# Performance work log

Hardware: AMD Instinct MI355X
Metric: run time of the kernel (lower is better)

The kernel has to match this reference:

```python
import jax, jax.numpy as jnp
import numpy as np

N_NODES = 50000


def gcn_conv(x, src, dst, W, b):
    # PyG GCNConv: h = x @ W; symmetric norm with added self-loops; out = A_hat h + b
    h = x @ W
    deg = jax.ops.segment_sum(jnp.ones_like(src, dtype=h.dtype), dst,
                              num_segments=N_NODES) + 1.0  # +1 self-loop
    dis = jax.lax.rsqrt(deg)  # deg >= 1, safe
    msg = h[src] * (dis[src] * dis[dst])[:, None]          # [E,H] gather + scale
    agg = jax.ops.segment_sum(msg, dst, num_segments=N_NODES)
    agg = agg + h * (dis * dis)[:, None]                   # self-loop contribution
    return agg + b


def link_pred(zs, e, Wp, bp):
    # zs: [L,N,H]; gather endpoints along node dim, per-edge cross-layer Gram matrix
    s = zs[:, e[0]]                                # [L,E,H]
    d = zs[:, e[1]]                                # [L,E,H]
    dot = jnp.einsum('leh,meh->elm', s, d)         # [E,L,L] per-edge bmm
    emb = dot.reshape(dot.shape[0], -1)            # [E,L*L]
    return emb @ Wp + bp                           # [E,1] logits (activation=False)


def reference(x, ei, pos, neg, W0, b0, Wh, bh, Wp, bp):
    src, dst = ei[0], ei[1]
    h = jax.nn.relu(gcn_conv(x, src, dst, W0, b0))
    embs = [h]
    for i in range(Wh.shape[0]):  # fixed small layer count
        h = jax.nn.relu(gcn_conv(h, src, dst, Wh[i], bh[i]))
        embs.append(h)
    zs = jnp.stack(embs, axis=0)                   # [L,N,H]
    pos_pred = link_pred(zs, pos, Wp, bp)
    neg_pred = link_pred(zs, neg, Wp, bp)
    logits = jnp.concatenate([pos_pred, neg_pred], axis=0)  # [2E,1]
    # faithful to source: targets all zero except row index == n_pos set to 1
    targets = jnp.zeros_like(logits).at[pos_pred.shape[0]].set(1.0)
    # BCEWithLogitsLoss (mean, numerically stable)
    loss = jnp.mean(jnp.clip(logits, 0.0) - logits * targets
                    + jnp.log1p(jnp.exp(-jnp.abs(logits))))
    return loss


def setup_inputs():
    key = jax.random.key(0)
    ks = jax.random.split(key, 10)
    N, E, EP, IN, H, L = 50000, 800000, 100000, 128, 64, 4
    x = jax.random.normal(ks[0], (N, IN), jnp.float32)
    ei = jax.random.randint(ks[1], (2, E), 0, N, dtype=jnp.int32)
    pos = jax.random.randint(ks[2], (2, EP), 0, N, dtype=jnp.int32)
    neg = jax.random.randint(ks[3], (2, EP), 0, N, dtype=jnp.int32)
    def u(k, shape, fan_in):
        s = 1.0 / np.sqrt(fan_in)
        return jax.random.uniform(k, shape, jnp.float32, -s, s)
    W0 = u(ks[4], (IN, H), IN)
    b0 = u(ks[5], (H,), IN)
    Wh = u(ks[6], (L - 1, H, H), H)
    bh = u(ks[7], (L - 1, H), H)
    Wp = u(ks[8], (L * L, 1), L * L)
    bp = u(ks[9], (1,), L * L)
    return {"x": x, "ei": ei, "pos": pos, "neg": neg, "W0": W0, "b0": b0,
            "Wh": Wh, "bh": bh, "Wp": Wp, "bp": bp}
```

## Files before the change

### kernel.cpp

```cpp
#include <hip/hip_runtime.h>
#include <hip/hip_bf16.h>
#include <math.h>

constexpr int N_NODES = 50000;
constexpr int HD = 64;
constexpr int NBKT = (N_NODES + 255) / 256;

typedef float floatx2 __attribute__((ext_vector_type(2)));

__device__ __forceinline__ float bf2f(unsigned short u) {
    return __uint_as_float((unsigned)u << 16);
}
__device__ __forceinline__ unsigned short f2bf(float f) {
    __hip_bfloat16 b = __float2bfloat16(f);
    return *(unsigned short*)&b;
}
__device__ __forceinline__ unsigned pack_fp8x4(float a, float b, float c, float d) {
    unsigned p = __builtin_amdgcn_cvt_pk_fp8_f32(a, b, 0u, false);
    return __builtin_amdgcn_cvt_pk_fp8_f32(c, d, p, true);
}
__device__ __forceinline__ float dot16_fp8(uint4 u, uint4 d) {
    const unsigned uu[4] = {u.x, u.y, u.z, u.w};
    const unsigned dd[4] = {d.x, d.y, d.z, d.w};
    float s = 0.f;
#pragma unroll
    for (int q = 0; q < 4; ++q) {
        floatx2 ua = __builtin_amdgcn_cvt_pk_f32_fp8(uu[q], false);
        floatx2 ub = __builtin_amdgcn_cvt_pk_f32_fp8(uu[q], true);
        floatx2 da = __builtin_amdgcn_cvt_pk_f32_fp8(dd[q], false);
        floatx2 db = __builtin_amdgcn_cvt_pk_f32_fp8(dd[q], true);
        s = fmaf(ua[0], da[0], s);
        s = fmaf(ua[1], da[1], s);
        s = fmaf(ub[0], db[0], s);
        s = fmaf(ub[1], db[1], s);
    }
    return s;
}

__global__ __launch_bounds__(256) void gemm128_bhist_kernel(
        const float* __restrict__ in_, const float* __restrict__ W,
        unsigned short* __restrict__ out16, unsigned* __restrict__ out8,
        const int* __restrict__ dst, int* __restrict__ bcnt,
        int N, int E, int nGemm) {
    __shared__ float xs[64][68];
    __shared__ float Wl[64][64];
    const int t = threadIdx.x;
    if ((int)blockIdx.x >= nGemm) {
        int* lh = (int*)&xs[0][0];
        lh[t] = 0;
        __syncthreads();
        const int beg = ((int)blockIdx.x - nGemm) * 2048;
        const int end = min(beg + 2048, E);
        for (int i = beg + t; i < end; i += 256)
            atomicAdd(&lh[dst[i] >> 8], 1);
        __syncthreads();
        if (t < NBKT && lh[t]) atomicAdd(&bcnt[t], lh[t]);
        return;
    }
    constexpr int K = 128;
    const int row0 = blockIdx.x * 64;
    const int cq = t & 15, rq = t >> 4;
    float acc[4][4] = {{0.f}};
    for (int kc = 0; kc < K; kc += 64) {
#pragma unroll
        for (int it = 0; it < 4; ++it) {
            const int idx = it * 256 + t;
            const int r = idx >> 4, c4 = idx & 15;
            const int rr = min(row0 + r, N - 1);
            *(float4*)(&xs[r][c4 * 4]) = *(const float4*)(in_ + (size_t)rr * K + kc + c4 * 4);
            *(float4*)(&Wl[r][c4 * 4]) = *(const float4*)(W + (size_t)(kc + r) * HD + c4 * 4);
        }
        __syncthreads();
#pragma unroll
        for (int k4 = 0; k4 < 16; ++k4) {
            float a[4][4], b[4][4];
#pragma unroll
            for (int i = 0; i < 4; ++i)
                *(float4*)a[i] = *(const float4*)(&xs[rq * 4 + i][k4 * 4]);
#pragma unroll
            for (int kk = 0; kk < 4; ++kk)
                *(float4*)b[kk] = *(const float4*)(&Wl[k4 * 4 + kk][cq * 4]);
#pragma unroll
            for (int kk = 0; kk < 4; ++kk)
#pragma unroll
                for (int i = 0; i < 4; ++i)
#pragma unroll
                    for (int j = 0; j < 4; ++j)
                        acc[i][j] = fmaf(a[i][kk], b[kk][j], acc[i][j]);
        }
        __syncthreads();
    }
#pragma unroll
    for (int i = 0; i < 4; ++i) {
        const int r = row0 + rq * 4 + i;
        if (r < N) {
            ushort4 o;
            o.x = f2bf(acc[i][0]); o.y = f2bf(acc[i][1]);
            o.z = f2bf(acc[i][2]); o.w = f2bf(acc[i][3]);
            *(ushort4*)(out16 + (size_t)r * HD + cq * 4) = o;
            out8[(size_t)r * 16 + cq] = pack_fp8x4(acc[i][0], acc[i][1], acc[i][2], acc[i][3]);
        }
    }
}

__global__ __launch_bounds__(256) void bscan_kernel(const int* __restrict__ bcnt,
                                                    int* __restrict__ bbase,
                                                    int* __restrict__ gcur) {
    const int t = threadIdx.x;
    const int v = (t < NBKT) ? bcnt[t] : 0;
    const int lane = t & 63, wid = t >> 6;
    int incl = v;
#pragma unroll
    for (int o = 1; o <= 32; o <<= 1) {
        int u = __shfl_up(incl, o);
        if (lane >= o) incl += u;
    }
    __shared__ int wt[4];
    if (lane == 63) wt[wid] = incl;
    __syncthreads();
    int base = 0;
    for (int w = 0; w < wid; ++w) base += wt[w];
    const int excl = base + incl - v;
    if (t < NBKT) { bbase[t] = excl; gcur[t] = excl; }
    if (t == NBKT - 1) bbase[NBKT] = excl + v;
}

__global__ __launch_bounds__(256) void partition_kernel(const int* __restrict__ src,
                                                        const int* __restrict__ dst,
                                                        int* __restrict__ gcur,
                                                        unsigned* __restrict__ pk, int E) {
    __shared__ unsigned epk[8192];
    __shared__ int lh[NBKT], lbase[NBKT], lcur[NBKT];
    const int t = threadIdx.x;
    for (int i = t; i < NBKT; i += 256) { lh[i] = 0; lcur[i] = 0; }
    __syncthreads();
    const int beg = blockIdx.x * 8192;
    const int end = min(beg + 8192, E);
    for (int i = beg + t; i < end; i += 256) {
        const int s = src[i], d = dst[i];
        const int bkt = d >> 8;
        epk[i - beg] = ((unsigned)bkt << 24) | ((unsigned)(d & 255) << 16) | (unsigned)s;
        atomicAdd(&lh[bkt], 1);
    }
    __syncthreads();
    for (int i = t; i < NBKT; i += 256)
        if (lh[i]) lbase[i] = atomicAdd(&gcur[i], lh[i]);
    __syncthreads();
    for (int i = beg + t; i < end; i += 256) {
        const unsigned p = epk[i - beg];
        const int bkt = p >> 24;
        const int r = atomicAdd(&lcur[bkt], 1);
        pk[lbase[bkt] + r] = p;
    }
}

__global__ __launch_bounds__(256) void bsort_kernel(const unsigned* __restrict__ pk,
                                                    const int* __restrict__ bbase,
                                                    int* __restrict__ off,
                                                    float* __restrict__ dis,
                                                    int* __restrict__ csr, int E, int N) {
    __shared__ int ncnt[256], nbs[256], ncur[256];
    __shared__ int wt[4];
    const int t = threadIdx.x;
    const int bkt = blockIdx.x;
    const int gb = bbase[bkt], ge = bbase[bkt + 1];
    ncnt[t] = 0; ncur[t] = 0;
    __syncthreads();
    for (int i = gb + t; i < ge; i += 256)
        atomicAdd(&ncnt[(pk[i] >> 16) & 255], 1);
    __syncthreads();
    const int v = ncnt[t];
    const int lane = t & 63, wid = t >> 6;
    int incl = v;
#pragma unroll
    for (int o = 1; o <= 32; o <<= 1) {
        int u = __shfl_up(incl, o);
        if (lane >= o) incl += u;
    }
    if (lane == 63) wt[wid] = incl;
    __syncthreads();
    int base = 0;
    for (int w = 0; w < wid; ++w) base += wt[w];
    nbs[t] = base + incl - v;
    const int n = bkt * 256 + t;
    if (n < N) {
        off[n] = gb + nbs[t];
        dis[n] = rsqrtf((float)v + 1.0f);
        if (n == N - 1) off[N] = E;
    }
    __syncthreads();
    for (int i = gb + t; i < ge; i += 256) {
        const unsigned p = pk[i];
        const int dl = (p >> 16) & 255;
        const int r = atomicAdd(&ncur[dl], 1);
        csr[gb + nbs[dl] + r] = (int)(p & 0xFFFFu);
    }
}

__global__ __launch_bounds__(256) void gemm64_kernel(const unsigned short* __restrict__ in16,
                                                     const float* __restrict__ W,
                                                     unsigned short* __restrict__ out16,
                                                     unsigned* __restrict__ out8, int N) {
    constexpr int K = 64;
    __shared__ float xs[64][68];
    __shared__ float Wl[64][64];
    const int t = threadIdx.x;
    const int row0 = blockIdx.x * 64;
    const int cq = t & 15, rq = t >> 4;
    float acc[4][4] = {{0.f}};
    {
#pragma unroll
        for (int it = 0; it < 4; ++it) {
            const int idx = it * 256 + t;
            const int r = idx >> 4, c4 = idx & 15;
            const int rr = min(row0 + r, N - 1);
            const ushort4 v = *(const ushort4*)(in16 + (size_t)rr * K + c4 * 4);
            *(float4*)(&xs[r][c4 * 4]) = make_float4(bf2f(v.x), bf2f(v.y), bf2f(v.z), bf2f(v.w));
            *(float4*)(&Wl[r][c4 * 4]) = *(const float4*)(W + (size_t)r * HD + c4 * 4);
        }
        __syncthreads();
#pragma unroll
        for (int k4 = 0; k4 < 16; ++k4) {
            float a[4][4], b[4][4];
#pragma unroll
            for (int i = 0; i < 4; ++i)
                *(float4*)a[i] = *(const float4*)(&xs[rq * 4 + i][k4 * 4]);
#pragma unroll
            for (int kk = 0; kk < 4; ++kk)
                *(float4*)b[kk] = *(const float4*)(&Wl[k4 * 4 + kk][cq * 4]);
#pragma unroll
            for (int kk = 0; kk < 4; ++kk)
#pragma unroll
                for (int i = 0; i < 4; ++i)
#pragma unroll
                    for (int j = 0; j < 4; ++j)
                        acc[i][j] = fmaf(a[i][kk], b[kk][j], acc[i][j]);
        }
    }
#pragma unroll
    for (int i = 0; i < 4; ++i) {
        const int r = row0 + rq * 4 + i;
        if (r < N) {
            ushort4 o;
            o.x = f2bf(acc[i][0]); o.y = f2bf(acc[i][1]);
            o.z = f2bf(acc[i][2]); o.w = f2bf(acc[i][3]);
            *(ushort4*)(out16 + (size_t)r * HD + cq * 4) = o;
            out8[(size_t)r * 16 + cq] = pack_fp8x4(acc[i][0], acc[i][1], acc[i][2], acc[i][3]);
        }
    }
}

template <bool FINAL>
__global__ __launch_bounds__(256) void agg_kernel(const int* __restrict__ csr,
                                                  const int* __restrict__ off,
                                                  const float* __restrict__ dis,
                                                  const unsigned short* __restrict__ h16,
                                                  const unsigned* __restrict__ h8,
                                                  const float* __restrict__ b,
                                                  unsigned short* __restrict__ z16out,
                                                  const unsigned short* __restrict__ zall,
                                                  const float* __restrict__ Wp,
                                                  unsigned* __restrict__ u8,
                                                  unsigned* __restrict__ d8, int N) {
    const int lane = threadIdx.x & 63;
    const int wid  = threadIdx.x >> 6;
    const int n = blockIdx.x * 4 + wid;
    if (n >= N) return;
    const int beg = off[n];
    const int c = min(off[n + 1] - beg, 64);
    int   s_l = 0;
    float w_l = 0.f;
    if (lane < c) {
        s_l = csr[beg + lane];
        w_l = dis[s_l];
    }
    const float dn = dis[n];
    const int g = lane >> 3;
    const int p = lane & 7;
    float a[8];
#pragma unroll
    for (int j = 0; j < 8; ++j) a[j] = 0.f;
    int   sE = __shfl(s_l, g);
    float wE = __shfl(w_l, g);
    uint2 hv = *(const uint2*)(h8 + (size_t)sE * 16 + p * 2);
    for (int e = 8; e < c; e += 8) {
        const int   sN = __shfl(s_l, e + g);
        const float wN = __shfl(w_l, e + g);
        const uint2 nv = *(const uint2*)(h8 + (size_t)sN * 16 + p * 2);
        floatx2 f01 = __builtin_amdgcn_cvt_pk_f32_fp8(hv.x, false);
        floatx2 f23 = __builtin_amdgcn_cvt_pk_f32_fp8(hv.x, true);
        floatx2 f45 = __builtin_amdgcn_cvt_pk_f32_fp8(hv.y, false);
        floatx2 f67 = __builtin_amdgcn_cvt_pk_f32_fp8(hv.y, true);
        a[0] = fmaf(f01[0], wE, a[0]); a[1] = fmaf(f01[1], wE, a[1]);
        a[2] = fmaf(f23[0], wE, a[2]); a[3] = fmaf(f23[1], wE, a[3]);
        a[4] = fmaf(f45[0], wE, a[4]); a[5] = fmaf(f45[1], wE, a[5]);
        a[6] = fmaf(f67[0], wE, a[6]); a[7] = fmaf(f67[1], wE, a[7]);
        hv = nv; wE = wN;
    }
    {
        floatx2 f01 = __builtin_amdgcn_cvt_pk_f32_fp8(hv.x, false);
        floatx2 f23 = __builtin_amdgcn_cvt_pk_f32_fp8(hv.x, true);
        floatx2 f45 = __builtin_amdgcn_cvt_pk_f32_fp8(hv.y, false);
        floatx2 f67 = __builtin_amdgcn_cvt_pk_f32_fp8(hv.y, true);
        a[0] = fmaf(f01[0], wE, a[0]); a[1] = fmaf(f01[1], wE, a[1]);
        a[2] = fmaf(f23[0], wE, a[2]); a[3] = fmaf(f23[1], wE, a[3]);
        a[4] = fmaf(f45[0], wE, a[4]); a[5] = fmaf(f45[1], wE, a[5]);
        a[6] = fmaf(f67[0], wE, a[6]); a[7] = fmaf(f67[1], wE, a[7]);
    }
#pragma unroll
    for (int st = 8; st <= 32; st <<= 1)
#pragma unroll
        for (int j = 0; j < 8; ++j) a[j] += __shfl_xor(a[j], st);
    if (g == 0) {
        const uint4 sv = *(const uint4*)(h16 + (size_t)n * HD + p * 8);
        const unsigned ss[4] = {sv.x, sv.y, sv.z, sv.w};
        const float4 b0 = *(const float4*)(b + p * 8);
        const float4 b1 = *(const float4*)(b + p * 8 + 4);
        const float bb[8] = {b0.x, b0.y, b0.z, b0.w, b1.x, b1.y, b1.z, b1.w};
        float o[8];
#pragma unroll
        for (int q = 0; q < 4; ++q) {
            o[2 * q]     = a[2 * q]     + __uint_as_float(ss[q] << 16) * dn;
            o[2 * q + 1] = a[2 * q + 1] + __uint_as_float(ss[q] & 0xFFFF0000u) * dn;
        }
        unsigned short z3b[8];
#pragma unroll
        for (int j = 0; j < 8; ++j) {
            const float v = fmaxf(fmaf(o[j], dn, bb[j]), 0.f);
            z3b[j] = f2bf(v);
        }
        unsigned short* zp = z16out + (size_t)n * HD + p * 8;
        *(ushort4*)zp = *(ushort4*)z3b;
        *(ushort4*)(zp + 4) = *(ushort4*)(z3b + 4);
        if constexpr (FINAL) {
            const size_t NH = (size_t)N_NODES * HD;
            const unsigned short* l0 = zall + 0 * NH + (size_t)n * HD + p * 8;
            const unsigned short* l1 = zall + 1 * NH + (size_t)n * HD + p * 8;
            const unsigned short* l2 = zall + 2 * NH + (size_t)n * HD + p * 8;
            unsigned short L0[8], L1[8], L2[8];
            *(ushort4*)L0 = *(const ushort4*)l0; *(ushort4*)(L0 + 4) = *(const ushort4*)(l0 + 4);
            *(ushort4*)L1 = *(const ushort4*)l1; *(ushort4*)(L1 + 4) = *(const ushort4*)(l1 + 4);
            *(ushort4*)L2 = *(const ushort4*)l2; *(ushort4*)(L2 + 4) = *(const ushort4*)(l2 + 4);
            float wpc[16];
#pragma unroll
            for (int m = 0; m < 16; ++m) wpc[m] = Wp[m];
            unsigned uo[8], dvo[8];
#pragma unroll
            for (int j = 0; j < 8; ++j) {
                const float v0 = bf2f(L0[j]), v1 = bf2f(L1[j]);
                const float v2 = bf2f(L2[j]), v3 = bf2f(z3b[j]);
                dvo[j] = pack_fp8x4(v0, v1, v2, v3);
                const float u0v = v0 * wpc[0] + v1 * wpc[4] + v2 * wpc[8]  + v3 * wpc[12];
                const float u1v = v0 * wpc[1] + v1 * wpc[5] + v2 * wpc[9]  + v3 * wpc[13];
                const float u2v = v0 * wpc[2] + v1 * wpc[6] + v2 * wpc[10] + v3 * wpc[14];
                const float u3v = v0 * wpc[3] + v1 * wpc[7] + v2 * wpc[11] + v3 * wpc[15];
                uo[j] = pack_fp8x4(u0v, u1v, u2v, u3v);
            }
            unsigned* up = u8 + (size_t)n * HD + p * 8;
            unsigned* dp = d8 + (size_t)n * HD + p * 8;
            *(uint4*)up = *(uint4*)uo;  *(uint4*)(up + 4) = *(uint4*)(uo + 4);
            *(uint4*)dp = *(uint4*)dvo; *(uint4*)(dp + 4) = *(uint4*)(dvo + 4);
        }
    }
}

__global__ __launch_bounds__(256) void linkpred_kernel(const unsigned* __restrict__ u8,
                                                       const unsigned* __restrict__ d8,
                                                       const int* __restrict__ pos,
                                                       const int* __restrict__ neg,
                                                       const float* __restrict__ bp,
                                                       double* __restrict__ acc, int EP) {
    const int lane = threadIdx.x & 63;
    const int wid  = threadIdx.x >> 6;
    const int grp  = lane >> 4;
    const int p    = lane & 15;
    const float bpv = bp[0];
    int gw = blockIdx.x * 4 + wid;
    const int nw = gridDim.x * 4;
    const int nchunks = (2 * EP) >> 3;
    float lsum = 0.f;
    for (int c0 = gw; c0 < nchunks; c0 += nw) {
        const int c = __builtin_amdgcn_readfirstlane(c0);
        const int i0 = c << 3;
        const bool is_pos = i0 < EP;
        const int* __restrict__ eptr = is_pos ? pos : neg;
        const int jj0 = is_pos ? i0 : i0 - EP;
        int idx = 0;
        if (lane < 16)
            idx = (lane < 8) ? eptr[jj0 + lane] : eptr[EP + jj0 + lane - 8];
        const int e0a = __shfl(idx, grp),     e1a = __shfl(idx, 8 + grp);
        const int e0b = __shfl(idx, 4 + grp), e1b = __shfl(idx, 12 + grp);
        const uint4 ua = *(const uint4*)(u8 + (size_t)e0a * HD + p * 4);
        const uint4 da = *(const uint4*)(d8 + (size_t)e1a * HD + p * 4);
        const uint4 ub = *(const uint4*)(u8 + (size_t)e0b * HD + p * 4);
        const uint4 db = *(const uint4*)(d8 + (size_t)e1b * HD + p * 4);
        float tA = dot16_fp8(ua, da);
        float tB = dot16_fp8(ub, db);
#pragma unroll
        for (int st = 1; st <= 8; st <<= 1) {
            tA += __shfl_xor(tA, st);
            tB += __shfl_xor(tB, st);
        }
        const float ga = __shfl(tA, (lane & 3) * 16);
        const float gb = __shfl(tB, (lane & 3) * 16);
        const float tt = (lane < 4) ? ga : gb;
        if (lane < 8) {
            float logit  = tt + bpv;
            float target = (i0 + lane == EP) ? 1.f : 0.f;
            lsum += fmaxf(logit, 0.f) - logit * target + log1pf(expf(-fabsf(logit)));
        }
    }
#pragma unroll
    for (int o = 32; o >= 1; o >>= 1) lsum += __shfl_xor(lsum, o);
    __shared__ float wsum[4];
    if (lane == 0) wsum[wid] = lsum;
    __syncthreads();
    if (threadIdx.x == 0) {
        double bs = (double)wsum[0] + (double)wsum[1] + (double)wsum[2] + (double)wsum[3];
        atomicAdd(acc, bs);
    }
}

__global__ void loss_final(const double* __restrict__ acc, float* __restrict__ out, int denom) {
    out[0] = (float)(acc[0] / (double)denom);
}

extern "C" void kernel_launch(void* const* d_in, const int* in_sizes, int n_in,
                              void* d_out, int out_size, void* d_ws, size_t ws_size,
                              hipStream_t stream) {
    const float* x   = (const float*)d_in[0];
    const int*   ei  = (const int*)d_in[1];
    const int*   pos = (const int*)d_in[2];
    const int*   neg = (const int*)d_in[3];
    const float* W0  = (const float*)d_in[4];
    const float* b0  = (const float*)d_in[5];
    const float* Wh  = (const float*)d_in[6];
    const float* bh  = (const float*)d_in[7];
    const float* Wp  = (const float*)d_in[8];
    const float* bp  = (const float*)d_in[9];
    const int E  = in_sizes[1] / 2;
    const int EP = in_sizes[2] / 2;
    const int N  = N_NODES;
    const size_t NH = (size_t)N * HD;

    char* ws = (char*)d_ws;
    size_t off_b = 0;
    auto alloc = [&](size_t bytes) { char* p = ws + off_b; off_b = (off_b + bytes + 255) & ~(size_t)255; return p; };
    unsigned short* h16 = (unsigned short*)alloc(NH * sizeof(unsigned short));
    unsigned*       h8  = (unsigned*)alloc(NH);
    unsigned short* z16 = (unsigned short*)alloc(4 * NH * sizeof(unsigned short));
    unsigned*       u8  = (unsigned*)alloc(NH * sizeof(unsigned));
    unsigned*       d8  = (unsigned*)alloc(NH * sizeof(unsigned));
    float* dis = (float*)alloc((size_t)N * sizeof(float));
    int*   off = (int*)alloc((size_t)(N + 1) * sizeof(int));
    int*   csr = (int*)alloc((size_t)E * sizeof(int));
    unsigned* pk = (unsigned*)alloc((size_t)E * sizeof(unsigned));
    int*   bbase = (int*)alloc((size_t)(NBKT + 1) * sizeof(int));
    int*   gcur  = (int*)alloc((size_t)NBKT * sizeof(int));
    char*  zbase = ws + off_b;
    int*   bcnt = (int*)alloc((size_t)NBKT * sizeof(int));
    double* acc = (double*)alloc(sizeof(double));
    size_t zero_bytes = (size_t)((char*)acc - zbase) + sizeof(double);

    hipMemsetAsync(zbase, 0, zero_bytes, stream);

    const int* src = ei;
    const int* dst = ei + E;

    const int gemm_blocks = (N + 63) / 64;
    const int bhist_blocks = (E + 2047) / 2048;
    const int agg_blocks  = (N + 3) / 4;

    gemm128_bhist_kernel<<<gemm_blocks + bhist_blocks, 256, 0, stream>>>(
        x, W0, h16, h8, dst, bcnt, N, E, gemm_blocks);
    bscan_kernel<<<1, 256, 0, stream>>>(bcnt, bbase, gcur);
    partition_kernel<<<(E + 8191) / 8192, 256, 0, stream>>>(src, dst, gcur, pk, E);
    bsort_kernel<<<NBKT, 256, 0, stream>>>(pk, bbase, off, dis, csr, E, N);

    agg_kernel<false><<<agg_blocks, 256, 0, stream>>>(csr, off, dis, h16, h8, b0,
                                                      z16, z16, Wp, u8, d8, N);

    for (int l = 1; l < 4; ++l) {
        unsigned short* zprev = z16 + (size_t)(l - 1) * NH;
        unsigned short* zcur  = z16 + (size_t)l * NH;
        gemm64_kernel<<<gemm_blocks, 256, 0, stream>>>(zprev, Wh + (size_t)(l - 1) * HD * HD, h16, h8, N);
        if (l < 3) {
            agg_kernel<false><<<agg_blocks, 256, 0, stream>>>(csr, off, dis, h16, h8,
                                                              bh + (size_t)(l - 1) * HD,
                                                              zcur, z16, Wp, u8, d8, N);
        } else {
            agg_kernel<true><<<agg_blocks, 256, 0, stream>>>(csr, off, dis, h16, h8,
                                                             bh + (size_t)(l - 1) * HD,
                                                             zcur, z16, Wp, u8, d8, N);
        }
    }

    linkpred_kernel<<<2048, 256, 0, stream>>>(u8, d8, pos, neg, bp, acc, EP);
    loss_final<<<1, 1, 0, stream>>>(acc, (float*)d_out, 2 * EP);
}
```

Before: 274.5 us.

## Pre-scale GEMM outputs by source degree norm and drop bf16 feature copy

The GEMM epilogues now multiply each row by dis[r] before packing to fp8, so aggregation becomes a plain sum and no longer loads a per-edge dis[src] weight or shuffles it. The self-loop term is read from the same fp8 buffer instead of a separate bf16 copy, which removes that buffer's writes and reads. A zeroed sentinel row N replaces masked lanes. The first GEMM is split out of the histogram kernel and moved after the CSR build so it can read dis, losing the overlap between GEMM and histogram and lowering self-loop precision to fp8.

After: 287.0 us. +4.6%, slower.

```diff
diff --git a/kernel.cpp b/kernel.cpp
--- a/kernel.cpp
+++ b/kernel.cpp
@@ -37,70 +37,18 @@
     return s;
 }
 
-__global__ __launch_bounds__(256) void gemm128_bhist_kernel(
-        const float* __restrict__ in_, const float* __restrict__ W,
-        unsigned short* __restrict__ out16, unsigned* __restrict__ out8,
-        const int* __restrict__ dst, int* __restrict__ bcnt,
-        int N, int E, int nGemm) {
-    __shared__ float xs[64][68];
-    __shared__ float Wl[64][64];
-    const int t = threadIdx.x;
-    if ((int)blockIdx.x >= nGemm) {
-        int* lh = (int*)&xs[0][0];
-        lh[t] = 0;
-        __syncthreads();
-        const int beg = ((int)blockIdx.x - nGemm) * 2048;
-        const int end = min(beg + 2048, E);
-        for (int i = beg + t; i < end; i += 256)
-            atomicAdd(&lh[dst[i] >> 8], 1);
-        __syncthreads();
-        if (t < NBKT && lh[t]) atomicAdd(&bcnt[t], lh[t]);
-        return;
-    }
-    constexpr int K = 128;
-    const int row0 = blockIdx.x * 64;
-    const int cq = t & 15, rq = t >> 4;
-    float acc[4][4] = {{0.f}};
-    for (int kc = 0; kc < K; kc += 64) {
-#pragma unroll
-        for (int it = 0; it < 4; ++it) {
-            const int idx = it * 256 + t;
-            const int r = idx >> 4, c4 = idx & 15;
-            const int rr = min(row0 + r, N - 1);
-            *(float4*)(&xs[r][c4 * 4]) = *(const float4*)(in_ + (size_t)rr * K + kc + c4 * 4);
-            *(float4*)(&Wl[r][c4 * 4]) = *(const float4*)(W + (size_t)(kc + r) * HD + c4 * 4);
-        }
-        __syncthreads();
-#pragma unroll
-        for (int k4 = 0; k4 < 16; ++k4) {
-            float a[4][4], b[4][4];
-#pragma unroll
-            for (int i = 0; i < 4; ++i)
-                *(float4*)a[i] = *(const float4*)(&xs[rq * 4 + i][k4 * 4]);
-#pragma unroll
-            for (int kk = 0; kk < 4; ++kk)
-                *(float4*)b[kk] = *(const float4*)(&Wl[k4 * 4 + kk][cq * 4]);
-#pragma unroll
-            for (int kk = 0; kk < 4; ++kk)
-#pragma unroll
-                for (int i = 0; i < 4; ++i)
-#pragma unroll
-                    for (int j = 0; j < 4; ++j)
-                        acc[i][j] = fmaf(a[i][kk], b[kk][j], acc[i][j]);
-        }
-        __syncthreads();
-    }
-#pragma unroll
-    for (int i = 0; i < 4; ++i) {
-        const int r = row0 + rq * 4 + i;
-        if (r < N) {
-            ushort4 o;
-            o.x = f2bf(acc[i][0]); o.y = f2bf(acc[i][1]);
-            o.z = f2bf(acc[i][2]); o.w = f2bf(acc[i][3]);
-            *(ushort4*)(out16 + (size_t)r * HD + cq * 4) = o;
-            out8[(size_t)r * 16 + cq] = pack_fp8x4(acc[i][0], acc[i][1], acc[i][2], acc[i][3]);
-        }
-    }
+__global__ __launch_bounds__(256) void bhist_kernel(const int* __restrict__ dst,
+                                                    int* __restrict__ bcnt, int E) {
+    __shared__ int lh[256];
+    const int t = threadIdx.x;
+    lh[t] = 0;
+    __syncthreads();
+    const int beg = blockIdx.x * 2048;
+    const int end = min(beg + 2048, E);
+    for (int i = beg + t; i < end; i += 256)
+        atomicAdd(&lh[dst[i] >> 8], 1);
+    __syncthreads();
+    if (t < NBKT && lh[t]) atomicAdd(&bcnt[t], lh[t]);
 }
 
 __global__ __launch_bounds__(256) void bscan_kernel(const int* __restrict__ bcnt,
@@ -197,9 +145,60 @@
     }
 }
 
+__global__ __launch_bounds__(256) void gemm128_kernel(const float* __restrict__ in_,
+                                                      const float* __restrict__ W,
+                                                      const float* __restrict__ dis,
+                                                      unsigned* __restrict__ out8, int N) {
+    constexpr int K = 128;
+    __shared__ float xs[64][68];
+    __shared__ float Wl[64][64];
+    const int t = threadIdx.x;
+    const int row0 = blockIdx.x * 64;
+    const int cq = t & 15, rq = t >> 4;
+    float acc[4][4] = {{0.f}};
+    for (int kc = 0; kc < K; kc += 64) {
+#pragma unroll
+        for (int it = 0; it < 4; ++it) {
+            const int idx = it * 256 + t;
+            const int r = idx >> 4, c4 = idx & 15;
+            const int rr = min(row0 + r, N - 1);
+            *(float4*)(&xs[r][c4 * 4]) = *(const float4*)(in_ + (size_t)rr * K + kc + c4 * 4);
+            *(float4*)(&Wl[r][c4 * 4]) = *(const float4*)(W + (size_t)(kc + r) * HD + c4 * 4);
+        }
+        __syncthreads();
+#pragma unroll
+        for (int k4 = 0; k4 < 16; ++k4) {
+            float a[4][4], b[4][4];
+#pragma unroll
+            for (int i = 0; i < 4; ++i)
+                *(float4*)a[i] = *(const float4*)(&xs[rq * 4 + i][k4 * 4]);
+#pragma unroll
+            for (int kk = 0; kk < 4; ++kk)
+                *(float4*)b[kk] = *(const float4*)(&Wl[k4 * 4 + kk][cq * 4]);
+#pragma unroll
+            for (int kk = 0; kk < 4; ++kk)
+#pragma unroll
+                for (int i = 0; i < 4; ++i)
+#pragma unroll
+                    for (int j = 0; j < 4; ++j)
+                        acc[i][j] = fmaf(a[i][kk], b[kk][j], acc[i][j]);
+        }
+        __syncthreads();
+    }
+#pragma unroll
+    for (int i = 0; i < 4; ++i) {
+        const int r = row0 + rq * 4 + i;
+        if (r < N) {
+            const float dr = dis[r];
+            out8[(size_t)r * 16 + cq] =
+                pack_fp8x4(acc[i][0] * dr, acc[i][1] * dr, acc[i][2] * dr, acc[i][3] * dr);
+        }
+    }
+}
+
 __global__ __launch_bounds__(256) void gemm64_kernel(const unsigned short* __restrict__ in16,
                                                      const float* __restrict__ W,
-                                                     unsigned short* __restrict__ out16,
+                                                     const float* __restrict__ dis,
                                                      unsigned* __restrict__ out8, int N) {
     constexpr int K = 64;
     __shared__ float xs[64][68];
@@ -241,11 +240,9 @@
     for (int i = 0; i < 4; ++i) {
         const int r = row0 + rq * 4 + i;
         if (r < N) {
-            ushort4 o;
-            o.x = f2bf(acc[i][0]); o.y = f2bf(acc[i][1]);
-            o.z = f2bf(acc[i][2]); o.w = f2bf(acc[i][3]);
-            *(ushort4*)(out16 + (size_t)r * HD + cq * 4) = o;
-            out8[(size_t)r * 16 + cq] = pack_fp8x4(acc[i][0], acc[i][1], acc[i][2], acc[i][3]);
+            const float dr = dis[r];
+            out8[(size_t)r * 16 + cq] =
+                pack_fp8x4(acc[i][0] * dr, acc[i][1] * dr, acc[i][2] * dr, acc[i][3] * dr);
         }
     }
 }
@@ -254,8 +251,7 @@
 __global__ __launch_bounds__(256) void agg_kernel(const int* __restrict__ csr,
                                                   const int* __restrict__ off,
                                                   const float* __restrict__ dis,
-                                                  const unsigned short* __restrict__ h16,
-                                                  const unsigned* __restrict__ h8,
+                                                  const unsigned* __restrict__ hs,
                                                   const float* __restrict__ b,
                                                   unsigned short* __restrict__ z16out,
                                                   const unsigned short* __restrict__ zall,
@@ -268,65 +264,54 @@
     if (n >= N) return;
     const int beg = off[n];
     const int c = min(off[n + 1] - beg, 64);
-    int   s_l = 0;
-    float w_l = 0.f;
-    if (lane < c) {
-        s_l = csr[beg + lane];
-        w_l = dis[s_l];
-    }
+    int s_l = N;
+    if (lane < c) s_l = csr[beg + lane];
     const float dn = dis[n];
     const int g = lane >> 3;
     const int p = lane & 7;
     float a[8];
 #pragma unroll
     for (int j = 0; j < 8; ++j) a[j] = 0.f;
-    int   sE = __shfl(s_l, g);
-    float wE = __shfl(w_l, g);
-    uint2 hv = *(const uint2*)(h8 + (size_t)sE * 16 + p * 2);
+    int sE = __shfl(s_l, g);
+    uint2 hv = *(const uint2*)(hs + (size_t)sE * 16 + p * 2);
     for (int e = 8; e < c; e += 8) {
-        const int   sN = __shfl(s_l, e + g);
-        const float wN = __shfl(w_l, e + g);
-        const uint2 nv = *(const uint2*)(h8 + (size_t)sN * 16 + p * 2);
+        const int sN = __shfl(s_l, e + g);
+        const uint2 nv = *(const uint2*)(hs + (size_t)sN * 16 + p * 2);
         floatx2 f01 = __builtin_amdgcn_cvt_pk_f32_fp8(hv.x, false);
         floatx2 f23 = __builtin_amdgcn_cvt_pk_f32_fp8(hv.x, true);
         floatx2 f45 = __builtin_amdgcn_cvt_pk_f32_fp8(hv.y, false);
         floatx2 f67 = __builtin_amdgcn_cvt_pk_f32_fp8(hv.y, true);
-        a[0] = fmaf(f01[0], wE, a[0]); a[1] = fmaf(f01[1], wE, a[1]);
-        a[2] = fmaf(f23[0], wE, a[2]); a[3] = fmaf(f23[1], wE, a[3]);
-        a[4] = fmaf(f45[0], wE, a[4]); a[5] = fmaf(f45[1], wE, a[5]);
-        a[6] = fmaf(f67[0], wE, a[6]); a[7] = fmaf(f67[1], wE, a[7]);
-        hv = nv; wE = wN;
+        a[0] += f01[0]; a[1] += f01[1]; a[2] += f23[0]; a[3] += f23[1];
+        a[4] += f45[0]; a[5] += f45[1]; a[6] += f67[0]; a[7] += f67[1];
+        hv = nv;
     }
     {
         floatx2 f01 = __builtin_amdgcn_cvt_pk_f32_fp8(hv.x, false);
         floatx2 f23 = __builtin_amdgcn_cvt_pk_f32_fp8(hv.x, true);
         floatx2 f45 = __builtin_amdgcn_cvt_pk_f32_fp8(hv.y, false);
         floatx2 f67 = __builtin_amdgcn_cvt_pk_f32_fp8(hv.y, true);
-        a[0] = fmaf(f01[0], wE, a[0]); a[1] = fmaf(f01[1], wE, a[1]);
-        a[2] = fmaf(f23[0], wE, a[2]); a[3] = fmaf(f23[1], wE, a[3]);
-        a[4] = fmaf(f45[0], wE, a[4]); a[5] = fmaf(f45[1], wE, a[5]);
-        a[6] = fmaf(f67[0], wE, a[6]); a[7] = fmaf(f67[1], wE, a[7]);
+        a[0] += f01[0]; a[1] += f01[1]; a[2] += f23[0]; a[3] += f23[1];
+        a[4] += f45[0]; a[5] += f45[1]; a[6] += f67[0]; a[7] += f67[1];
     }
 #pragma unroll
     for (int st = 8; st <= 32; st <<= 1)
 #pragma unroll
         for (int j = 0; j < 8; ++j) a[j] += __shfl_xor(a[j], st);
     if (g == 0) {
-        const uint4 sv = *(const uint4*)(h16 + (size_t)n * HD + p * 8);
-        const unsigned ss[4] = {sv.x, sv.y, sv.z, sv.w};
+        const uint2 sv = *(const uint2*)(hs + (size_t)n * 16 + p * 2);
+        floatx2 s01 = __builtin_amdgcn_cvt_pk_f32_fp8(sv.x, false);
+        floatx2 s23 = __builtin_amdgcn_cvt_pk_f32_fp8(sv.x, true);
+        floatx2 s45 = __builtin_amdgcn_cvt_pk_f32_fp8(sv.y, false);
+        floatx2 s67 = __builtin_amdgcn_cvt_pk_f32_fp8(sv.y, true);
+        a[0] += s01[0]; a[1] += s01[1]; a[2] += s23[0]; a[3] += s23[1];
+        a[4] += s45[0]; a[5] += s45[1]; a[6] += s67[0]; a[7] += s67[1];
         const float4 b0 = *(const float4*)(b + p * 8);
         const float4 b1 = *(const float4*)(b + p * 8 + 4);
         const float bb[8] = {b0.x, b0.y, b0.z, b0.w, b1.x, b1.y, b1.z, b1.w};
-        float o[8];
-#pragma unroll
-        for (int q = 0; q < 4; ++q) {
-            o[2 * q]     = a[2 * q]     + __uint_as_float(ss[q] << 16) * dn;
-            o[2 * q + 1] = a[2 * q + 1] + __uint_as_float(ss[q] & 0xFFFF0000u) * dn;
-        }
         unsigned short z3b[8];
 #pragma unroll
         for (int j = 0; j < 8; ++j) {
-            const float v = fmaxf(fmaf(o[j], dn, bb[j]), 0.f);
+            const float v = fmaxf(fmaf(a[j], dn, bb[j]), 0.f);
             z3b[j] = f2bf(v);
         }
         unsigned short* zp = z16out + (size_t)n * HD + p * 8;
@@ -446,8 +431,7 @@
     char* ws = (char*)d_ws;
     size_t off_b = 0;
     auto alloc = [&](size_t bytes) { char* p = ws + off_b; off_b = (off_b + bytes + 255) & ~(size_t)255; return p; };
-    unsigned short* h16 = (unsigned short*)alloc(NH * sizeof(unsigned short));
-    unsigned*       h8  = (unsigned*)alloc(NH);
+    unsigned*       hs  = (unsigned*)alloc((size_t)(N + 1) * 16 * sizeof(unsigned));
     unsigned short* z16 = (unsigned short*)alloc(4 * NH * sizeof(unsigned short));
     unsigned*       u8  = (unsigned*)alloc(NH * sizeof(unsigned));
     unsigned*       d8  = (unsigned*)alloc(NH * sizeof(unsigned));
@@ -463,33 +447,34 @@
     size_t zero_bytes = (size_t)((char*)acc - zbase) + sizeof(double);
 
     hipMemsetAsync(zbase, 0, zero_bytes, stream);
+    hipMemsetAsync(hs + (size_t)N * 16, 0, 16 * sizeof(unsigned), stream);
 
     const int* src = ei;
     const int* dst = ei + E;
 
-    const int gemm_blocks = (N + 63) / 64;
-    const int bhist_blocks = (E + 2047) / 2048;
-    const int agg_blocks  = (N + 3) / 4;
-
-    gemm128_bhist_kernel<<<gemm_blocks + bhist_blocks, 256, 0, stream>>>(
-        x, W0, h16, h8, dst, bcnt, N, E, gemm_blocks);
+    bhist_kernel<<<(E + 2047) / 2048, 256, 0, stream>>>(dst, bcnt, E);
     bscan_kernel<<<1, 256, 0, stream>>>(bcnt, bbase, gcur);
     partition_kernel<<<(E + 8191) / 8192, 256, 0, stream>>>(src, dst, gcur, pk, E);
     bsort_kernel<<<NBKT, 256, 0, stream>>>(pk, bbase, off, dis, csr, E, N);
 
-    agg_kernel<false><<<agg_blocks, 256, 0, stream>>>(csr, off, dis, h16, h8, b0,
+    const int gemm_blocks = (N + 63) / 64;
+    const int agg_blocks  = (N + 3) / 4;
+
+    gemm128_kernel<<<gemm_blocks, 256, 0, stream>>>(x, W0, dis, hs, N);
+    agg_kernel<false><<<agg_blocks, 256, 0, stream>>>(csr, off, dis, hs, b0,
                                                       z16, z16, Wp, u8, d8, N);
 
     for (int l = 1; l < 4; ++l) {
         unsigned short* zprev = z16 + (size_t)(l - 1) * NH;
         unsigned short* zcur  = z16 + (size_t)l * NH;
-        gemm64_kernel<<<gemm_blocks, 256, 0, stream>>>(zprev, Wh + (size_t)(l - 1) * HD * HD, h16, h8, N);
+        gemm64_kernel<<<gemm_blocks, 256, 0, stream>>>(zprev, Wh + (size_t)(l - 1) * HD * HD,
+                                                       dis, hs, N);
         if (l < 3) {
-            agg_kernel<false><<<agg_blocks, 256, 0, stream>>>(csr, off, dis, h16, h8,
+            agg_kernel<false><<<agg_blocks, 256, 0, stream>>>(csr, off, dis, hs,
                                                               bh + (size_t)(l - 1) * HD,
                                                               zcur, z16, Wp, u8, d8, N);
         } else {
-            agg_kernel<true><<<agg_blocks, 256, 0, stream>>>(csr, off, dis, h16, h8,
+            agg_kernel<true><<<agg_blocks, 256, 0, stream>>>(csr, off, dis, hs,
                                                              bh + (size_t)(l - 1) * HD,
                                                              zcur, z16, Wp, u8, d8, N);
         }
```
